# Kernel optimization log

Hardware: AMD Instinct MI355X
Metric: run time of the kernel (lower is better)

Reference implementation:

```python
import jax, jax.numpy as jnp
import numpy as np

H = 8  # num_heads
EPS = 1e-5


def _lin_params(key, din, dout, scale=0.02):
    kw, _ = jax.random.split(key)
    W = jax.random.normal(kw, (din, dout), jnp.float32) * scale
    b = jnp.zeros((dout,), jnp.float32)
    return W, b


def _edge_attention(x_src, x_dst, ei, ea, Wq, bq, Wk, bk, Wv, bv, We, be, Wo, bo, n_dst):
    out_c = Wq.shape[1]
    D = out_c // H
    scale = D ** -0.5
    q = (x_dst @ Wq + bq).reshape(-1, H, D)
    k = (x_src @ Wk + bk).reshape(-1, H, D)
    v = (x_src @ Wv + bv).reshape(-1, H, D)
    e = (ea @ We + be).reshape(-1, H, D)
    src, dst = ei[0], ei[1]
    ke = k[src] + e                                # [E,H,D]
    ve = v[src] + e                                # [E,H,D]
    s = jnp.einsum('ehd,ehd->eh', q[dst], ke) * scale  # [E,H]
    # segment (per-destination) softmax, numerically stable
    m = jax.ops.segment_max(s, dst, num_segments=n_dst)
    ex = jnp.exp(s - m[dst])
    den = jax.ops.segment_sum(ex, dst, num_segments=n_dst)
    a = ex / den[dst]                              # [E,H]  (dropout = identity in eval)
    agg = jax.ops.segment_sum(a[..., None] * ve, dst, num_segments=n_dst)  # [N_dst,H,D]
    return agg.reshape(n_dst, out_c) @ Wo + bo


def _layernorm(x, g, b):
    mu = jnp.mean(x, axis=-1, keepdims=True)
    var = jnp.mean((x - mu) ** 2, axis=-1, keepdims=True)
    return (x - mu) * jax.lax.rsqrt(var + EPS) * g + b


def setup_inputs() -> dict:
    key = jax.random.key(0)
    ks = jax.random.split(key, 32)
    N_pc, N_gr, E_pp, E_pg = 50000, 8000, 400000, 100000
    din, dout, de = 128, 128, 64
    inp = {}
    inp['x_pc'] = jax.random.normal(ks[0], (N_pc, din), jnp.float32)
    inp['x_gr'] = jax.random.normal(ks[1], (N_gr, din), jnp.float32)
    inp['ea_pp'] = jax.random.normal(ks[2], (E_pp, de), jnp.float32)
    inp['ea_pg'] = jax.random.normal(ks[3], (E_pg, de), jnp.float32)
    inp['ei_pp'] = jax.random.randint(ks[4], (2, E_pp), 0, N_pc, jnp.int32)
    src_pg = jax.random.randint(ks[5], (E_pg,), 0, N_pc, jnp.int32)
    dst_pg = jax.random.randint(ks[6], (E_pg,), 0, N_gr, jnp.int32)
    inp['ei_pg'] = jnp.stack([src_pg, dst_pg])
    i = 7
    for et in ('pp', 'pg'):
        for nm, d_in in (('Wq', din), ('Wk', din), ('Wv', din), ('We', de), ('Wo', dout)):
            W, b = _lin_params(ks[i], d_in, dout); i += 1
            inp[f'{nm}_{et}'] = W
            inp[f'b{nm[1].lower()}_{et}'] = b
    for nt, d_in in (('pc', din), ('gr', din)):
        W, b = _lin_params(ks[i], d_in, dout); i += 1
        inp[f'Wnp_{nt}'] = W
        inp[f'bnp_{nt}'] = b
        inp[f'g_{nt}'] = jnp.ones((dout,), jnp.float32)
        inp[f'bln_{nt}'] = jnp.zeros((dout,), jnp.float32)
    return inp


def reference(x_pc, x_gr, ea_pp, ea_pg, ei_pp, ei_pg,
              Wq_pp, bq_pp, Wk_pp, bk_pp, Wv_pp, bv_pp, We_pp, be_pp, Wo_pp, bo_pp,
              Wq_pg, bq_pg, Wk_pg, bk_pg, Wv_pg, bv_pg, We_pg, be_pg, Wo_pg, bo_pg,
              Wnp_pc, bnp_pc, Wnp_gr, bnp_gr, g_pc, bln_pc, g_gr, bln_gr):
    N_pc, N_gr = x_pc.shape[0], x_gr.shape[0]
    out_pc = x_pc @ Wnp_pc + bnp_pc
    out_gr = x_gr @ Wnp_gr + bnp_gr
    out_pc = out_pc + _edge_attention(x_pc, x_pc, ei_pp, ea_pp,
                                      Wq_pp, bq_pp, Wk_pp, bk_pp, Wv_pp, bv_pp,
                                      We_pp, be_pp, Wo_pp, bo_pp, N_pc)
    out_gr = out_gr + _edge_attention(x_pc, x_gr, ei_pg, ea_pg,
                                      Wq_pg, bq_pg, Wk_pg, bk_pg, Wv_pg, bv_pg,
                                      We_pg, be_pg, Wo_pg, bo_pg, N_gr)
    out_pc = _layernorm(out_pc, g_pc, bln_pc)
    out_gr = _layernorm(out_gr, g_gr, bln_gr)
    return out_pc, out_gr
```

## Files before the change

### kernel.cpp

```cpp
#include <hip/hip_runtime.h>
#include <hip/hip_bf16.h>
#include <stdint.h>

typedef short short8 __attribute__((ext_vector_type(8)));
typedef float f32x4 __attribute__((ext_vector_type(4)));

__device__ __forceinline__ unsigned short f2bf(float x) {
    unsigned u = __float_as_uint(x);
    u += 0x7fffu + ((u >> 16) & 1u);
    return (unsigned short)(u >> 16);
}
__device__ __forceinline__ float bflo(unsigned u) { return __uint_as_float(u << 16); }
__device__ __forceinline__ float bfhi(unsigned u) { return __uint_as_float(u & 0xffff0000u); }

struct WDesc { const float* src; unsigned short* dst; int K, ldd, koff, perm; };
struct WPack { WDesc w[12]; };

__global__ __launch_bounds__(256) void prep_and_count(WPack p,
        const int* __restrict__ d0, int E0, int* c0,
        const int* __restrict__ d1, int E1, int* c1, int nPrep) {
    if ((int)blockIdx.x < nPrep) {
        int wi = blockIdx.x >> 2, chunk = blockIdx.x & 3;
        WDesc d = p.w[wi];
        int total = d.K * 128, cs = total >> 2;
        int lo = chunk * cs, hi = lo + cs;
        for (int i = lo + threadIdx.x; i < hi; i += 256) {
            int n = i / d.K, k = i - n * d.K;
            int kk = d.perm ? (2 * (k & 63) + (k >> 6)) : k;
            d.dst[(size_t)n * d.ldd + d.koff + kk] = f2bf(d.src[(size_t)k * 128 + n]);
        }
    } else {
        int t = (blockIdx.x - nPrep) * 256 + threadIdx.x;
        if (t < E0) atomicAdd(&c0[d0[t]], 1);
        else if (t < E0 + E1) atomicAdd(&c1[d1[t - E0]], 1);
    }
}

struct NodeOut { const unsigned short* Wt; const float* bias; unsigned int* out; int ldc, coloff; };
struct NodePack { NodeOut d[5]; int nout; };

__global__ __launch_bounds__(256) void gemm_node(const float* __restrict__ A0, int M0, NodePack p0,
                                                 int B0,
                                                 const float* __restrict__ A1, int M1, NodePack p1) {
    constexpr int K = 128, LDA = 136, LDB = 72, TLD = 133;
    __shared__ __align__(16) unsigned short As[64 * LDA];
    __shared__ __align__(16) unsigned short Bs[128 * LDB];

    const float* A; int M; NodePack dp; int blk;
    if ((int)blockIdx.x < B0) { A = A0; M = M0; dp = p0; blk = blockIdx.x; }
    else { A = A1; M = M1; dp = p1; blk = blockIdx.x - B0; }

    const int tid = threadIdx.x;
    const int rbase = blk * 64;

    for (int slot = tid; slot < 64 * 16; slot += 256) {
        int row = slot >> 4, kg = slot & 15;
        int gr = rbase + row;
        short8 s8 = {0, 0, 0, 0, 0, 0, 0, 0};
        if (gr < M) {
            const float* a = A + (size_t)gr * K + kg * 8;
            float4 f0 = *reinterpret_cast<const float4*>(a);
            float4 f1 = *reinterpret_cast<const float4*>(a + 4);
            s8[0] = (short)f2bf(f0.x); s8[1] = (short)f2bf(f0.y);
            s8[2] = (short)f2bf(f0.z); s8[3] = (short)f2bf(f0.w);
            s8[4] = (short)f2bf(f1.x); s8[5] = (short)f2bf(f1.y);
            s8[6] = (short)f2bf(f1.z); s8[7] = (short)f2bf(f1.w);
        }
        *reinterpret_cast<short8*>(&As[row * LDA + kg * 8]) = s8;
    }

    const int lane = tid & 63, w = tid >> 6;
    const int rb = (w >> 1) * 32, cb = (w & 1) * 64;
    const int qd = lane >> 4, l16 = lane & 15;

    for (int o = 0; o < dp.nout; ++o) {
        NodeOut d = dp.d[o];
        f32x4 acc[2][4];
#pragma unroll
        for (int rt = 0; rt < 2; ++rt)
#pragma unroll
            for (int ct = 0; ct < 4; ++ct) { f32x4 z = {0.f,0.f,0.f,0.f}; acc[rt][ct] = z; }

        for (int kc = 0; kc < K; kc += 64) {
            __syncthreads();
            for (int slot = tid; slot < 128 * 8; slot += 256) {
                int n = slot >> 3, kg = slot & 7;
                *reinterpret_cast<short8*>(&Bs[n * LDB + kg * 8]) =
                    *reinterpret_cast<const short8*>(d.Wt + (size_t)n * K + kc + kg * 8);
            }
            __syncthreads();
#pragma unroll
            for (int ks = 0; ks < 64; ks += 32) {
                short8 af[2], bfr[4];
#pragma unroll
                for (int rt = 0; rt < 2; ++rt)
                    af[rt] = *reinterpret_cast<const short8*>(
                        &As[(rb + rt * 16 + l16) * LDA + kc + ks + qd * 8]);
#pragma unroll
                for (int ct = 0; ct < 4; ++ct)
                    bfr[ct] = *reinterpret_cast<const short8*>(
                        &Bs[(cb + ct * 16 + l16) * LDB + ks + qd * 8]);
#pragma unroll
                for (int rt = 0; rt < 2; ++rt)
#pragma unroll
                    for (int ct = 0; ct < 4; ++ct)
                        acc[rt][ct] = __builtin_amdgcn_mfma_f32_16x16x32_bf16(
                            af[rt], bfr[ct], acc[rt][ct], 0, 0, 0);
            }
        }

        __syncthreads();
        unsigned short* tile = Bs;
#pragma unroll
        for (int ct = 0; ct < 4; ++ct) {
            int col = cb + ct * 16 + l16;
            float bv = d.bias[col];
#pragma unroll
            for (int rt = 0; rt < 2; ++rt)
#pragma unroll
                for (int r = 0; r < 4; ++r)
                    tile[(rb + rt * 16 + qd * 4 + r) * TLD + col] = f2bf(acc[rt][ct][r] + bv);
        }
        __syncthreads();
#pragma unroll
        for (int rep = 0; rep < 4; ++rep) {
            int lrow = (tid >> 4) + rep * 16, seg = tid & 15;
            int gr = rbase + lrow;
            if (gr < M) {
                uint4 pk;
#pragma unroll
                for (int j = 0; j < 4; ++j) {
                    int pcol = seg * 4 + j;
                    unsigned lo16 = tile[lrow * TLD + pcol];
                    unsigned hi16 = tile[lrow * TLD + pcol + 64];
                    ((unsigned*)&pk)[j] = lo16 | (hi16 << 16);
                }
                *reinterpret_cast<uint4*>(&d.out[(size_t)gr * d.ldc + d.coloff + seg * 4]) = pk;
            }
        }
    }
}

struct EdgePack {
    const float* A; const unsigned short* Wt; const float* bias;
    const int* pos; unsigned int* out; int M;
};

__global__ __launch_bounds__(256) void gemm_edge(EdgePack p0, EdgePack p1, int B0) {
    constexpr int LDB = 72;
    __shared__ __align__(16) unsigned short Bs[128 * LDB];

    EdgePack p; int blk;
    if ((int)blockIdx.x < B0) { p = p0; blk = blockIdx.x; } else { p = p1; blk = blockIdx.x - B0; }

    const int tid = threadIdx.x;
    for (int slot = tid; slot < 128 * 8; slot += 256) {
        int n = slot >> 3, k8 = slot & 7;
        *reinterpret_cast<short8*>(&Bs[n * LDB + k8 * 8]) =
            *reinterpret_cast<const short8*>(p.Wt + (size_t)n * 64 + k8 * 8);
    }
    __syncthreads();

    const int lane = tid & 63, w = tid >> 6;
    const int qd = lane >> 4, l16 = lane & 15;
    const int rbase = blk * 128 + w * 32;
    if (rbase >= p.M) return;

    float4 fa[4][2];
#pragma unroll
    for (int rt = 0; rt < 2; ++rt)
#pragma unroll
        for (int ks = 0; ks < 2; ++ks) {
            int gr = rbase + rt * 16 + l16;
            int grc = gr < p.M ? gr : p.M - 1;
            const float* a = p.A + (size_t)grc * 64 + ks * 32 + qd * 8;
            fa[rt * 2 + ks][0] = *reinterpret_cast<const float4*>(a);
            fa[rt * 2 + ks][1] = *reinterpret_cast<const float4*>(a + 4);
        }

    short8 af[2][2];
#pragma unroll
    for (int rt = 0; rt < 2; ++rt)
#pragma unroll
        for (int ks = 0; ks < 2; ++ks) {
            float4 f0 = fa[rt * 2 + ks][0], f1 = fa[rt * 2 + ks][1];
            short8 s;
            s[0] = (short)f2bf(f0.x); s[1] = (short)f2bf(f0.y);
            s[2] = (short)f2bf(f0.z); s[3] = (short)f2bf(f0.w);
            s[4] = (short)f2bf(f1.x); s[5] = (short)f2bf(f1.y);
            s[6] = (short)f2bf(f1.z); s[7] = (short)f2bf(f1.w);
            af[rt][ks] = s;
        }

    f32x4 acc[2][8];
#pragma unroll
    for (int rt = 0; rt < 2; ++rt)
#pragma unroll
        for (int ct = 0; ct < 8; ++ct) { f32x4 z = {0.f,0.f,0.f,0.f}; acc[rt][ct] = z; }
#pragma unroll
    for (int ks = 0; ks < 2; ++ks)
#pragma unroll
        for (int ct = 0; ct < 8; ++ct) {
            short8 bf = *reinterpret_cast<const short8*>(
                &Bs[(ct * 16 + l16) * LDB + ks * 32 + qd * 8]);
            acc[0][ct] = __builtin_amdgcn_mfma_f32_16x16x32_bf16(af[0][ks], bf, acc[0][ct], 0, 0, 0);
            acc[1][ct] = __builtin_amdgcn_mfma_f32_16x16x32_bf16(af[1][ks], bf, acc[1][ct], 0, 0, 0);
        }

    float blo[4], bhi[4];
#pragma unroll
    for (int ct = 0; ct < 4; ++ct) {
        blo[ct] = p.bias[ct * 16 + l16];
        bhi[ct] = p.bias[64 + ct * 16 + l16];
    }
#pragma unroll
    for (int rt = 0; rt < 2; ++rt)
#pragma unroll
        for (int r = 0; r < 4; ++r) {
            int gr = rbase + rt * 16 + qd * 4 + r;
            if (gr < p.M) {
                int dpos = p.pos[gr];
                unsigned int* dst = p.out + (size_t)dpos * 64 + l16;
#pragma unroll
                for (int ct = 0; ct < 4; ++ct) {
                    unsigned lo = f2bf(acc[rt][ct][r] + blo[ct]);
                    unsigned hi = f2bf(acc[rt][ct + 4][r] + bhi[ct]);
                    dst[ct * 16] = lo | (hi << 16);
                }
            }
        }
}

struct OutPack {
    const unsigned short* Aagg; const float* Ax;
    const unsigned short* Wt;
    const float *bo, *bnp, *g, *bln; float* out; int M;
};

__global__ __launch_bounds__(256) void gemm_out_ln(OutPack p0, OutPack p1, int B0) {
    constexpr int K = 256, LDA = 264, LDB = 72, FTLD = 132;
    __shared__ __align__(16) char smemA[64 * LDA * 2];
    __shared__ __align__(16) unsigned short Bs[128 * LDB];
    unsigned short* As = (unsigned short*)smemA;

    OutPack p; int blk;
    if ((int)blockIdx.x < B0) { p = p0; blk = blockIdx.x; } else { p = p1; blk = blockIdx.x - B0; }

    const int tid = threadIdx.x;
    const int rbase = blk * 64;

    for (int slot = tid; slot < 64 * 32; slot += 256) {
        int row = slot >> 5, kg = slot & 31;
        int gr = rbase + row;
        short8 s8 = {0, 0, 0, 0, 0, 0, 0, 0};
        if (gr < p.M) {
            if (kg < 16) {
                s8 = *reinterpret_cast<const short8*>(p.Aagg + (size_t)gr * 128 + kg * 8);
            } else {
                const float* a = p.Ax + (size_t)gr * 128 + (kg - 16) * 8;
                float4 f0 = *reinterpret_cast<const float4*>(a);
                float4 f1 = *reinterpret_cast<const float4*>(a + 4);
                s8[0] = (short)f2bf(f0.x); s8[1] = (short)f2bf(f0.y);
                s8[2] = (short)f2bf(f0.z); s8[3] = (short)f2bf(f0.w);
                s8[4] = (short)f2bf(f1.x); s8[5] = (short)f2bf(f1.y);
                s8[6] = (short)f2bf(f1.z); s8[7] = (short)f2bf(f1.w);
            }
        }
        *reinterpret_cast<short8*>(&As[row * LDA + kg * 8]) = s8;
    }

    const int lane = tid & 63, w = tid >> 6;
    const int rb = (w >> 1) * 32, cb = (w & 1) * 64;
    const int qd = lane >> 4, l16 = lane & 15;

    f32x4 acc[2][4];
#pragma unroll
    for (int rt = 0; rt < 2; ++rt)
#pragma unroll
        for (int ct = 0; ct < 4; ++ct) { f32x4 z = {0.f,0.f,0.f,0.f}; acc[rt][ct] = z; }

    for (int kc = 0; kc < K; kc += 64) {
        __syncthreads();
        for (int slot = tid; slot < 128 * 8; slot += 256) {
            int n = slot >> 3, kg = slot & 7;
            *reinterpret_cast<short8*>(&Bs[n * LDB + kg * 8]) =
                *reinterpret_cast<const short8*>(p.Wt + (size_t)n * K + kc + kg * 8);
        }
        __syncthreads();
#pragma unroll
        for (int ks = 0; ks < 64; ks += 32) {
            short8 af[2], bfr[4];
#pragma unroll
            for (int rt = 0; rt < 2; ++rt)
                af[rt] = *reinterpret_cast<const short8*>(
                    &As[(rb + rt * 16 + l16) * LDA + kc + ks + qd * 8]);
#pragma unroll
            for (int ct = 0; ct < 4; ++ct)
                bfr[ct] = *reinterpret_cast<const short8*>(
                    &Bs[(cb + ct * 16 + l16) * LDB + ks + qd * 8]);
#pragma unroll
            for (int rt = 0; rt < 2; ++rt)
#pragma unroll
                for (int ct = 0; ct < 4; ++ct)
                    acc[rt][ct] = __builtin_amdgcn_mfma_f32_16x16x32_bf16(
                        af[rt], bfr[ct], acc[rt][ct], 0, 0, 0);
        }
    }

    __syncthreads();
    float* ftile = (float*)smemA;
#pragma unroll
    for (int ct = 0; ct < 4; ++ct) {
        int col = cb + ct * 16 + l16;
        float bv = p.bo[col] + p.bnp[col];
#pragma unroll
        for (int rt = 0; rt < 2; ++rt)
#pragma unroll
            for (int r = 0; r < 4; ++r)
                ftile[(rb + rt * 16 + qd * 4 + r) * FTLD + col] = acc[rt][ct][r] + bv;
    }
    __syncthreads();

    int r = tid >> 2, q4 = tid & 3;
    const float* rowp = &ftile[r * FTLD + q4 * 32];
    float s = 0.f, sq = 0.f;
#pragma unroll
    for (int j = 0; j < 8; ++j) {
        float4 v = *reinterpret_cast<const float4*>(rowp + j * 4);
        s += v.x + v.y + v.z + v.w;
        sq += v.x * v.x + v.y * v.y + v.z * v.z + v.w * v.w;
    }
    s += __shfl_xor(s, 1, 64);  s += __shfl_xor(s, 2, 64);
    sq += __shfl_xor(sq, 1, 64); sq += __shfl_xor(sq, 2, 64);
    float mu = s * (1.f / 128.f);
    float var = sq * (1.f / 128.f) - mu * mu;
    float rs = rsqrtf(var + 1e-5f);
    int gr = rbase + r;
    if (gr < p.M) {
#pragma unroll
        for (int j = 0; j < 8; ++j) {
            float4 v = *reinterpret_cast<const float4*>(rowp + j * 4);
            int c = q4 * 32 + j * 4;
            float4 gg = *reinterpret_cast<const float4*>(p.g + c);
            float4 bb = *reinterpret_cast<const float4*>(p.bln + c);
            float4 o;
            o.x = (v.x - mu) * rs * gg.x + bb.x;
            o.y = (v.y - mu) * rs * gg.y + bb.y;
            o.z = (v.z - mu) * rs * gg.z + bb.z;
            o.w = (v.w - mu) * rs * gg.w + bb.w;
            *reinterpret_cast<float4*>(&p.out[(size_t)gr * 128 + c]) = o;
        }
    }
}

__global__ __launch_bounds__(1024) void scan_partial(const int* c0, int N0, int* rp0, int* bs0, int B0,
                                                     const int* c1, int N1, int* rp1, int* bs1) {
    __shared__ int wsum[16];
    const int* c; int* rp; int* bs; int N; int blk;
    if ((int)blockIdx.x < B0) { c = c0; rp = rp0; bs = bs0; N = N0; blk = blockIdx.x; }
    else { c = c1; rp = rp1; bs = bs1; N = N1; blk = blockIdx.x - B0; }
    int tid = threadIdx.x, lane = tid & 63, w = tid >> 6;
    int i = blk * 1024 + tid;
    int v = (i < N) ? c[i] : 0;
    int s = v;
#pragma unroll
    for (int off = 1; off < 64; off <<= 1) {
        int t = __shfl_up(s, off, 64);
        if (lane >= off) s += t;
    }
    if (lane == 63) wsum[w] = s;
    __syncthreads();
    if (w == 0 && lane < 16) {
        int ws = wsum[lane];
#pragma unroll
        for (int off = 1; off < 16; off <<= 1) {
            int t = __shfl_up(ws, off, 64);
            if (lane >= off) ws += t;
        }
        wsum[lane] = ws;
    }
    __syncthreads();
    int wexcl = (w == 0) ? 0 : wsum[w - 1];
    if (i < N) rp[i] = wexcl + s - v;
    if (tid == 0) bs[blk] = wsum[15];
}

__global__ __launch_bounds__(128) void scan_mid(const int* bs0, int* off0, int B0, int* rpN0,
                                                const int* bs1, int* off1, int B1, int* rpN1) {
    int w = threadIdx.x >> 6, lane = threadIdx.x & 63;
    const int* bs = w ? bs1 : bs0;
    int* off = w ? off1 : off0;
    int B = w ? B1 : B0;
    int* rpN = w ? rpN1 : rpN0;
    int v = (lane < B) ? bs[lane] : 0;
    int s = v;
#pragma unroll
    for (int o = 1; o < 64; o <<= 1) {
        int t = __shfl_up(s, o, 64);
        if (lane >= o) s += t;
    }
    if (lane < B) off[lane] = s - v;
    int total = __shfl(s, B - 1, 64);
    if (lane == 0) *rpN = total;
}

__global__ __launch_bounds__(1024) void scan_add(int* rp0, int* cur0, const int* off0, int N0, int B0,
                                                 int* rp1, int* cur1, const int* off1, int N1) {
    int* rp; int* cur; const int* off; int N; int blk;
    if ((int)blockIdx.x < B0) { rp = rp0; cur = cur0; off = off0; N = N0; blk = blockIdx.x; }
    else { rp = rp1; cur = cur1; off = off1; N = N1; blk = blockIdx.x - B0; }
    int i = blk * 1024 + threadIdx.x;
    if (i < N) {
        int vv = rp[i] + off[blk];
        rp[i] = vv;
        cur[i] = vv;
    }
}

__global__ __launch_bounds__(256) void scatter_both(
    const int* __restrict__ s0, const int* __restrict__ d0, int E0, int* cur0, int* pos0, int* srcs0,
    const int* __restrict__ s1, const int* __restrict__ d1, int E1, int* cur1, int* pos1, int* srcs1) {
    int t = blockIdx.x * 256 + threadIdx.x;
    if (t < E0) {
        int p = atomicAdd(&cur0[d0[t]], 1);
        pos0[t] = p;
        srcs0[p] = s0[t];
    } else if (t < E0 + E1) {
        int tt = t - E0;
        int p = atomicAdd(&cur1[d1[tt]], 1);
        pos1[tt] = p;
        srcs1[p] = s1[tt];
    }
}

struct AttnPack {
    const unsigned int *q, *kv, *e;
    const int *srcs;
    const int *row_ptr;
    unsigned int* agg; int N;
};

__global__ __launch_bounds__(256) void attn_gather(AttnPack a0, AttnPack a1, int B0) {
    AttnPack a; int blk;
    if ((int)blockIdx.x < B0) { a = a0; blk = blockIdx.x; } else { a = a1; blk = blockIdx.x - B0; }
    int dst = blk * 4 + (threadIdx.x >> 6);
    if (dst >= a.N) return;
    int lane = threadIdx.x & 63;

    unsigned qp = a.q[(size_t)dst * 64 + lane];
    float qlo = bflo(qp), qhi = bfhi(qp);
    int beg = a.row_ptr[dst], end = a.row_ptr[dst + 1];
    float denl = 0.f, denh = 0.f, accl = 0.f, acch = 0.f;

    int s0 = a.srcs[beg], s1 = a.srcs[beg + 1];
    unsigned k0 = a.kv[(size_t)s0 * 128 + lane];
    unsigned v0 = a.kv[(size_t)s0 * 128 + 64 + lane];
    unsigned e0 = a.e[(size_t)beg * 64 + lane];
    unsigned k1 = a.kv[(size_t)s1 * 128 + lane];
    unsigned v1 = a.kv[(size_t)s1 * 128 + 64 + lane];
    unsigned e1 = a.e[(size_t)(beg + 1) * 64 + lane];

    for (int i = beg; i < end; i += 2) {
        int sn0 = a.srcs[i + 2], sn1 = a.srcs[i + 3];
        unsigned kn0 = a.kv[(size_t)sn0 * 128 + lane];
        unsigned vn0 = a.kv[(size_t)sn0 * 128 + 64 + lane];
        unsigned en0 = a.e[(size_t)(i + 2) * 64 + lane];
        unsigned kn1 = a.kv[(size_t)sn1 * 128 + lane];
        unsigned vn1 = a.kv[(size_t)sn1 * 128 + 64 + lane];
        unsigned en1 = a.e[(size_t)(i + 3) * 64 + lane];

        float e0l = bflo(e0), e0h = bfhi(e0);
        float e1l = bflo(e1), e1h = bfhi(e1);
        float p0l = qlo * (bflo(k0) + e0l), p0h = qhi * (bfhi(k0) + e0h);
        float p1l = qlo * (bflo(k1) + e1l), p1h = qhi * (bfhi(k1) + e1h);
#pragma unroll
        for (int m = 1; m < 16; m <<= 1) {
            p0l += __shfl_xor(p0l, m, 64);
            p0h += __shfl_xor(p0h, m, 64);
            p1l += __shfl_xor(p1l, m, 64);
            p1h += __shfl_xor(p1h, m, 64);
        }
        float x0l = __expf(p0l * 0.25f), x0h = __expf(p0h * 0.25f);
        float x1l = __expf(p1l * 0.25f), x1h = __expf(p1h * 0.25f);
        bool second = (i + 1 < end);
        x1l = second ? x1l : 0.f;
        x1h = second ? x1h : 0.f;
        denl += x0l + x1l;
        denh += x0h + x1h;
        accl += x0l * (bflo(v0) + e0l) + x1l * (bflo(v1) + e1l);
        acch += x0h * (bfhi(v0) + e0h) + x1h * (bfhi(v1) + e1h);
        k0 = kn0; v0 = vn0; e0 = en0;
        k1 = kn1; v1 = vn1; e1 = en1;
    }
    float ol = denl > 0.f ? accl / denl : 0.f;
    float oh = denh > 0.f ? acch / denh : 0.f;
    a.agg[(size_t)dst * 64 + lane] = (unsigned)f2bf(ol) | ((unsigned)f2bf(oh) << 16);
}

extern "C" void kernel_launch(void* const* d_in, const int* in_sizes, int n_in,
                              void* d_out, int out_size, void* d_ws, size_t ws_size,
                              hipStream_t stream) {
    const float* x_pc  = (const float*)d_in[0];
    const float* x_gr  = (const float*)d_in[1];
    const float* ea_pp = (const float*)d_in[2];
    const float* ea_pg = (const float*)d_in[3];
    const int* ei_pp   = (const int*)d_in[4];
    const int* ei_pg   = (const int*)d_in[5];
    const float *Wq_pp = (const float*)d_in[6],  *bq_pp = (const float*)d_in[7];
    const float *Wk_pp = (const float*)d_in[8],  *bk_pp = (const float*)d_in[9];
    const float *Wv_pp = (const float*)d_in[10], *bv_pp = (const float*)d_in[11];
    const float *We_pp = (const float*)d_in[12], *be_pp = (const float*)d_in[13];
    const float *Wo_pp = (const float*)d_in[14], *bo_pp = (const float*)d_in[15];
    const float *Wq_pg = (const float*)d_in[16], *bq_pg = (const float*)d_in[17];
    const float *Wk_pg = (const float*)d_in[18], *bk_pg = (const float*)d_in[19];
    const float *Wv_pg = (const float*)d_in[20], *bv_pg = (const float*)d_in[21];
    const float *We_pg = (const float*)d_in[22], *be_pg = (const float*)d_in[23];
    const float *Wo_pg = (const float*)d_in[24], *bo_pg = (const float*)d_in[25];
    const float *Wnp_pc = (const float*)d_in[26], *bnp_pc = (const float*)d_in[27];
    const float *g_pc   = (const float*)d_in[28], *bln_pc = (const float*)d_in[29];
    const float *Wnp_gr = (const float*)d_in[30], *bnp_gr = (const float*)d_in[31];
    const float *g_gr   = (const float*)d_in[32], *bln_gr = (const float*)d_in[33];

    const int N_pc = in_sizes[0] / 128;
    const int N_gr = in_sizes[1] / 128;
    const int E_pp = in_sizes[4] / 2;
    const int E_pg = in_sizes[5] / 2;

    char* ws = (char*)d_ws;
    size_t off = 0;
    auto alloc = [&](size_t bytes) -> char* {
        char* p = ws + off;
        off += (bytes + 255) & ~(size_t)255;
        return p;
    };
    unsigned short* Wt_q_pp = (unsigned short*)alloc(128 * 128 * 2);
    unsigned short* Wt_k_pp = (unsigned short*)alloc(128 * 128 * 2);
    unsigned short* Wt_v_pp = (unsigned short*)alloc(128 * 128 * 2);
    unsigned short* Wt_k_pg = (unsigned short*)alloc(128 * 128 * 2);
    unsigned short* Wt_v_pg = (unsigned short*)alloc(128 * 128 * 2);
    unsigned short* Wt_q_pg = (unsigned short*)alloc(128 * 128 * 2);
    unsigned short* Wt_e_pp = (unsigned short*)alloc(64 * 128 * 2);
    unsigned short* Wt_e_pg = (unsigned short*)alloc(64 * 128 * 2);
    unsigned short* Wt_cat_pp = (unsigned short*)alloc(256 * 128 * 2);
    unsigned short* Wt_cat_gr = (unsigned short*)alloc(256 * 128 * 2);

    unsigned int* q_pp  = (unsigned int*)alloc((size_t)N_pc * 64 * 4);
    unsigned int* kv_pp = (unsigned int*)alloc((size_t)N_pc * 128 * 4);
    unsigned int* q_pg  = (unsigned int*)alloc((size_t)N_gr * 64 * 4);
    unsigned int* kv_pg = (unsigned int*)alloc((size_t)N_pc * 128 * 4);
    unsigned int* e_pp  = (unsigned int*)alloc((size_t)(E_pp + 4) * 64 * 4);
    unsigned int* e_pg  = (unsigned int*)alloc((size_t)(E_pg + 4) * 64 * 4);
    unsigned int* agg_pp = (unsigned int*)alloc((size_t)N_pc * 64 * 4);
    unsigned int* agg_pg = (unsigned int*)alloc((size_t)N_gr * 64 * 4);
    int* row_ptr_pp = (int*)alloc((size_t)(N_pc + 1) * 4);
    int* cursor_pp  = (int*)alloc((size_t)N_pc * 4);
    int* pos_pp     = (int*)alloc((size_t)E_pp * 4);
    int* row_ptr_pg = (int*)alloc((size_t)(N_gr + 1) * 4);
    int* cursor_pg  = (int*)alloc((size_t)N_gr * 4);
    int* pos_pg     = (int*)alloc((size_t)E_pg * 4);
    int* bsum_pp    = (int*)alloc(64 * 4);
    int* boff_pp    = (int*)alloc(64 * 4);
    int* bsum_pg    = (int*)alloc(64 * 4);
    int* boff_pg    = (int*)alloc(64 * 4);
    char* zbase = ws + off;
    int* counts_pp = (int*)alloc((size_t)N_pc * 4);
    int* counts_pg = (int*)alloc((size_t)N_gr * 4);
    int* srcs_pp   = (int*)alloc((size_t)(E_pp + 8) * 4);
    int* srcs_pg   = (int*)alloc((size_t)(E_pg + 8) * 4);
    size_t zbytes = (size_t)((ws + off) - zbase);
    hipMemsetAsync(zbase, 0, zbytes, stream);
    hipMemsetAsync(e_pp + (size_t)E_pp * 64, 0, 4 * 64 * 4, stream);
    hipMemsetAsync(e_pg + (size_t)E_pg * 64, 0, 4 * 64 * 4, stream);

    float* out_pc = (float*)d_out;
    float* out_gr = out_pc + (size_t)N_pc * 128;

    const int* src_pp = ei_pp;
    const int* dst_pp = ei_pp + E_pp;
    const int* src_pg = ei_pg;
    const int* dst_pg = ei_pg + E_pg;

    WPack wp;
    wp.w[0]  = {Wq_pp, Wt_q_pp, 128, 128, 0, 0};
    wp.w[1]  = {Wk_pp, Wt_k_pp, 128, 128, 0, 0};
    wp.w[2]  = {Wv_pp, Wt_v_pp, 128, 128, 0, 0};
    wp.w[3]  = {Wk_pg, Wt_k_pg, 128, 128, 0, 0};
    wp.w[4]  = {Wv_pg, Wt_v_pg, 128, 128, 0, 0};
    wp.w[5]  = {Wq_pg, Wt_q_pg, 128, 128, 0, 0};
    wp.w[6]  = {We_pp, Wt_e_pp, 64, 64, 0, 0};
    wp.w[7]  = {We_pg, Wt_e_pg, 64, 64, 0, 0};
    wp.w[8]  = {Wo_pp, Wt_cat_pp, 128, 256, 0, 1};
    wp.w[9]  = {Wnp_pc, Wt_cat_pp, 128, 256, 128, 0};
    wp.w[10] = {Wo_pg, Wt_cat_gr, 128, 256, 0, 1};
    wp.w[11] = {Wnp_gr, Wt_cat_gr, 128, 256, 128, 0};
    const int NPREP = 48;
    const int gE = (E_pp + E_pg + 255) / 256;
    prep_and_count<<<NPREP + gE, 256, 0, stream>>>(wp, dst_pp, E_pp, counts_pp,
                                                   dst_pg, E_pg, counts_pg, NPREP);

    const int Bs_pp = (N_pc + 1023) / 1024, Bs_pg = (N_gr + 1023) / 1024;
    scan_partial<<<Bs_pp + Bs_pg, 1024, 0, stream>>>(counts_pp, N_pc, row_ptr_pp, bsum_pp, Bs_pp,
                                                     counts_pg, N_gr, row_ptr_pg, bsum_pg);
    scan_mid<<<1, 128, 0, stream>>>(bsum_pp, boff_pp, Bs_pp, &row_ptr_pp[N_pc],
                                    bsum_pg, boff_pg, Bs_pg, &row_ptr_pg[N_gr]);
    scan_add<<<Bs_pp + Bs_pg, 1024, 0, stream>>>(row_ptr_pp, cursor_pp, boff_pp, N_pc, Bs_pp,
                                                 row_ptr_pg, cursor_pg, boff_pg, N_gr);
    scatter_both<<<gE, 256, 0, stream>>>(src_pp, dst_pp, E_pp, cursor_pp, pos_pp, srcs_pp,
                                         src_pg, dst_pg, E_pg, cursor_pg, pos_pg, srcs_pg);

    NodePack np;
    np.d[0] = {Wt_q_pp, bq_pp, q_pp, 64, 0};
    np.d[1] = {Wt_k_pp, bk_pp, kv_pp, 128, 0};
    np.d[2] = {Wt_v_pp, bv_pp, kv_pp, 128, 64};
    np.d[3] = {Wt_k_pg, bk_pg, kv_pg, 128, 0};
    np.d[4] = {Wt_v_pg, bv_pg, kv_pg, 128, 64};
    np.nout = 5;
    NodePack ng{};
    ng.d[0] = {Wt_q_pg, bq_pg, q_pg, 64, 0};
    ng.nout = 1;
    int Bn0 = (N_pc + 63) / 64, Bn1 = (N_gr + 63) / 64;
    gemm_node<<<Bn0 + Bn1, 256, 0, stream>>>(x_pc, N_pc, np, Bn0, x_gr, N_gr, ng);

    EdgePack ep0 = {ea_pp, Wt_e_pp, be_pp, pos_pp, e_pp, E_pp};
    EdgePack ep1 = {ea_pg, Wt_e_pg, be_pg, pos_pg, e_pg, E_pg};
    int Be0 = (E_pp + 127) / 128, Be1 = (E_pg + 127) / 128;
    gemm_edge<<<Be0 + Be1, 256, 0, stream>>>(ep0, ep1, Be0);

    AttnPack ap0 = {q_pp, kv_pp, e_pp, srcs_pp, row_ptr_pp, agg_pp, N_pc};
    AttnPack ap1 = {q_pg, kv_pg, e_pg, srcs_pg, row_ptr_pg, agg_pg, N_gr};
    int Ba0 = (N_pc + 3) / 4, Ba1 = (N_gr + 3) / 4;
    attn_gather<<<Ba0 + Ba1, 256, 0, stream>>>(ap0, ap1, Ba0);

    OutPack op0 = {(const unsigned short*)agg_pp, x_pc, Wt_cat_pp, bo_pp, bnp_pc, g_pc, bln_pc, out_pc, N_pc};
    OutPack op1 = {(const unsigned short*)agg_pg, x_gr, Wt_cat_gr, bo_pg, bnp_gr, g_gr, bln_gr, out_gr, N_gr};
    int Bo0 = (N_pc + 63) / 64, Bo1 = (N_gr + 63) / 64;
    gemm_out_ln<<<Bo0 + Bo1, 256, 0, stream>>>(op0, op1, Bo0);
}
```

Measured before the change: 523.7 us.

## Merge node and edge projection GEMMs into one launch without shared-memory staging

Replaces the separate node-projection and edge-projection kernels with a single kernel whose blocks are split between edge jobs and node jobs. Both paths now keep A fragments in registers and read bf16 weight fragments straight from global memory (cache) instead of staging them through LDS with barriers. The node path is retiled so each wave owns 32 rows across all 128 output columns. This removes a launch and the sync overhead and lets the two workloads overlap, at the cost of more register pressure and repeated global weight reads per wave, plus uncoalesced node output stores in place of the LDS-transposed vector stores.

```diff
diff --git a/kernel.cpp b/kernel.cpp
--- a/kernel.cpp
+++ b/kernel.cpp
@@ -36,199 +36,146 @@
     }
 }
 
-struct NodeOut { const unsigned short* Wt; const float* bias; unsigned int* out; int ldc, coloff; };
-struct NodePack { NodeOut d[5]; int nout; };
-
-__global__ __launch_bounds__(256) void gemm_node(const float* __restrict__ A0, int M0, NodePack p0,
-                                                 int B0,
-                                                 const float* __restrict__ A1, int M1, NodePack p1) {
-    constexpr int K = 128, LDA = 136, LDB = 72, TLD = 133;
-    __shared__ __align__(16) unsigned short As[64 * LDA];
-    __shared__ __align__(16) unsigned short Bs[128 * LDB];
-
-    const float* A; int M; NodePack dp; int blk;
-    if ((int)blockIdx.x < B0) { A = A0; M = M0; dp = p0; blk = blockIdx.x; }
-    else { A = A1; M = M1; dp = p1; blk = blockIdx.x - B0; }
-
-    const int tid = threadIdx.x;
-    const int rbase = blk * 64;
-
-    for (int slot = tid; slot < 64 * 16; slot += 256) {
-        int row = slot >> 4, kg = slot & 15;
-        int gr = rbase + row;
-        short8 s8 = {0, 0, 0, 0, 0, 0, 0, 0};
-        if (gr < M) {
-            const float* a = A + (size_t)gr * K + kg * 8;
-            float4 f0 = *reinterpret_cast<const float4*>(a);
-            float4 f1 = *reinterpret_cast<const float4*>(a + 4);
-            s8[0] = (short)f2bf(f0.x); s8[1] = (short)f2bf(f0.y);
-            s8[2] = (short)f2bf(f0.z); s8[3] = (short)f2bf(f0.w);
-            s8[4] = (short)f2bf(f1.x); s8[5] = (short)f2bf(f1.y);
-            s8[6] = (short)f2bf(f1.z); s8[7] = (short)f2bf(f1.w);
-        }
-        *reinterpret_cast<short8*>(&As[row * LDA + kg * 8]) = s8;
-    }
-
-    const int lane = tid & 63, w = tid >> 6;
-    const int rb = (w >> 1) * 32, cb = (w & 1) * 64;
-    const int qd = lane >> 4, l16 = lane & 15;
-
-    for (int o = 0; o < dp.nout; ++o) {
-        NodeOut d = dp.d[o];
-        f32x4 acc[2][4];
-#pragma unroll
-        for (int rt = 0; rt < 2; ++rt)
-#pragma unroll
-            for (int ct = 0; ct < 4; ++ct) { f32x4 z = {0.f,0.f,0.f,0.f}; acc[rt][ct] = z; }
-
-        for (int kc = 0; kc < K; kc += 64) {
-            __syncthreads();
-            for (int slot = tid; slot < 128 * 8; slot += 256) {
-                int n = slot >> 3, kg = slot & 7;
-                *reinterpret_cast<short8*>(&Bs[n * LDB + kg * 8]) =
-                    *reinterpret_cast<const short8*>(d.Wt + (size_t)n * K + kc + kg * 8);
-            }
-            __syncthreads();
-#pragma unroll
-            for (int ks = 0; ks < 64; ks += 32) {
-                short8 af[2], bfr[4];
-#pragma unroll
-                for (int rt = 0; rt < 2; ++rt)
-                    af[rt] = *reinterpret_cast<const short8*>(
-                        &As[(rb + rt * 16 + l16) * LDA + kc + ks + qd * 8]);
-#pragma unroll
-                for (int ct = 0; ct < 4; ++ct)
-                    bfr[ct] = *reinterpret_cast<const short8*>(
-                        &Bs[(cb + ct * 16 + l16) * LDB + ks + qd * 8]);
-#pragma unroll
-                for (int rt = 0; rt < 2; ++rt)
-#pragma unroll
-                    for (int ct = 0; ct < 4; ++ct)
-                        acc[rt][ct] = __builtin_amdgcn_mfma_f32_16x16x32_bf16(
-                            af[rt], bfr[ct], acc[rt][ct], 0, 0, 0);
-            }
-        }
-
-        __syncthreads();
-        unsigned short* tile = Bs;
-#pragma unroll
-        for (int ct = 0; ct < 4; ++ct) {
-            int col = cb + ct * 16 + l16;
-            float bv = d.bias[col];
-#pragma unroll
-            for (int rt = 0; rt < 2; ++rt)
-#pragma unroll
-                for (int r = 0; r < 4; ++r)
-                    tile[(rb + rt * 16 + qd * 4 + r) * TLD + col] = f2bf(acc[rt][ct][r] + bv);
-        }
-        __syncthreads();
-#pragma unroll
-        for (int rep = 0; rep < 4; ++rep) {
-            int lrow = (tid >> 4) + rep * 16, seg = tid & 15;
-            int gr = rbase + lrow;
-            if (gr < M) {
-                uint4 pk;
-#pragma unroll
-                for (int j = 0; j < 4; ++j) {
-                    int pcol = seg * 4 + j;
-                    unsigned lo16 = tile[lrow * TLD + pcol];
-                    unsigned hi16 = tile[lrow * TLD + pcol + 64];
-                    ((unsigned*)&pk)[j] = lo16 | (hi16 << 16);
-                }
-                *reinterpret_cast<uint4*>(&d.out[(size_t)gr * d.ldc + d.coloff + seg * 4]) = pk;
-            }
-        }
-    }
-}
-
-struct EdgePack {
+struct ProjDesc { const unsigned short* Wt; const float* bias; unsigned int* out; int ldc, coloff; };
+struct NodeJob { const float* A; int M; int nout; ProjDesc d[5]; };
+struct EdgeJob {
     const float* A; const unsigned short* Wt; const float* bias;
     const int* pos; unsigned int* out; int M;
 };
 
-__global__ __launch_bounds__(256) void gemm_edge(EdgePack p0, EdgePack p1, int B0) {
-    constexpr int LDB = 72;
-    __shared__ __align__(16) unsigned short Bs[128 * LDB];
-
-    EdgePack p; int blk;
-    if ((int)blockIdx.x < B0) { p = p0; blk = blockIdx.x; } else { p = p1; blk = blockIdx.x - B0; }
-
+__global__ __launch_bounds__(256) void gemm_ne(EdgeJob e0, EdgeJob e1, NodeJob n0, NodeJob n1,
+                                               int BE0, int BE1, int BN0) {
     const int tid = threadIdx.x;
-    for (int slot = tid; slot < 128 * 8; slot += 256) {
-        int n = slot >> 3, k8 = slot & 7;
-        *reinterpret_cast<short8*>(&Bs[n * LDB + k8 * 8]) =
-            *reinterpret_cast<const short8*>(p.Wt + (size_t)n * 64 + k8 * 8);
-    }
-    __syncthreads();
-
     const int lane = tid & 63, w = tid >> 6;
     const int qd = lane >> 4, l16 = lane & 15;
-    const int rbase = blk * 128 + w * 32;
-    if (rbase >= p.M) return;
-
-    float4 fa[4][2];
-#pragma unroll
-    for (int rt = 0; rt < 2; ++rt)
-#pragma unroll
-        for (int ks = 0; ks < 2; ++ks) {
-            int gr = rbase + rt * 16 + l16;
-            int grc = gr < p.M ? gr : p.M - 1;
-            const float* a = p.A + (size_t)grc * 64 + ks * 32 + qd * 8;
-            fa[rt * 2 + ks][0] = *reinterpret_cast<const float4*>(a);
-            fa[rt * 2 + ks][1] = *reinterpret_cast<const float4*>(a + 4);
-        }
-
-    short8 af[2][2];
-#pragma unroll
-    for (int rt = 0; rt < 2; ++rt)
-#pragma unroll
-        for (int ks = 0; ks < 2; ++ks) {
-            float4 f0 = fa[rt * 2 + ks][0], f1 = fa[rt * 2 + ks][1];
-            short8 s;
-            s[0] = (short)f2bf(f0.x); s[1] = (short)f2bf(f0.y);
-            s[2] = (short)f2bf(f0.z); s[3] = (short)f2bf(f0.w);
-            s[4] = (short)f2bf(f1.x); s[5] = (short)f2bf(f1.y);
-            s[6] = (short)f2bf(f1.z); s[7] = (short)f2bf(f1.w);
-            af[rt][ks] = s;
-        }
-
-    f32x4 acc[2][8];
-#pragma unroll
-    for (int rt = 0; rt < 2; ++rt)
-#pragma unroll
-        for (int ct = 0; ct < 8; ++ct) { f32x4 z = {0.f,0.f,0.f,0.f}; acc[rt][ct] = z; }
-#pragma unroll
-    for (int ks = 0; ks < 2; ++ks)
-#pragma unroll
-        for (int ct = 0; ct < 8; ++ct) {
-            short8 bf = *reinterpret_cast<const short8*>(
-                &Bs[(ct * 16 + l16) * LDB + ks * 32 + qd * 8]);
-            acc[0][ct] = __builtin_amdgcn_mfma_f32_16x16x32_bf16(af[0][ks], bf, acc[0][ct], 0, 0, 0);
-            acc[1][ct] = __builtin_amdgcn_mfma_f32_16x16x32_bf16(af[1][ks], bf, acc[1][ct], 0, 0, 0);
-        }
-
-    float blo[4], bhi[4];
-#pragma unroll
-    for (int ct = 0; ct < 4; ++ct) {
-        blo[ct] = p.bias[ct * 16 + l16];
-        bhi[ct] = p.bias[64 + ct * 16 + l16];
-    }
-#pragma unroll
-    for (int rt = 0; rt < 2; ++rt)
-#pragma unroll
-        for (int r = 0; r < 4; ++r) {
-            int gr = rbase + rt * 16 + qd * 4 + r;
-            if (gr < p.M) {
-                int dpos = p.pos[gr];
-                unsigned int* dst = p.out + (size_t)dpos * 64 + l16;
-#pragma unroll
-                for (int ct = 0; ct < 4; ++ct) {
-                    unsigned lo = f2bf(acc[rt][ct][r] + blo[ct]);
-                    unsigned hi = f2bf(acc[rt][ct + 4][r] + bhi[ct]);
-                    dst[ct * 16] = lo | (hi << 16);
+    int b = blockIdx.x;
+
+    if (b < BE0 + BE1) {
+        EdgeJob p; int blk;
+        if (b < BE0) { p = e0; blk = b; } else { p = e1; blk = b - BE0; }
+        const int rbase = blk * 128 + w * 32;
+        if (rbase >= p.M) return;
+
+        short8 af[2][2];
+#pragma unroll
+        for (int rt = 0; rt < 2; ++rt)
+#pragma unroll
+            for (int ks = 0; ks < 2; ++ks) {
+                int gr = rbase + rt * 16 + l16;
+                int grc = gr < p.M ? gr : p.M - 1;
+                const float* a = p.A + (size_t)grc * 64 + ks * 32 + qd * 8;
+                float4 f0 = *reinterpret_cast<const float4*>(a);
+                float4 f1 = *reinterpret_cast<const float4*>(a + 4);
+                short8 s;
+                s[0] = (short)f2bf(f0.x); s[1] = (short)f2bf(f0.y);
+                s[2] = (short)f2bf(f0.z); s[3] = (short)f2bf(f0.w);
+                s[4] = (short)f2bf(f1.x); s[5] = (short)f2bf(f1.y);
+                s[6] = (short)f2bf(f1.z); s[7] = (short)f2bf(f1.w);
+                af[rt][ks] = s;
+            }
+
+        f32x4 acc[2][8];
+#pragma unroll
+        for (int rt = 0; rt < 2; ++rt)
+#pragma unroll
+            for (int ct = 0; ct < 8; ++ct) { f32x4 z = {0.f,0.f,0.f,0.f}; acc[rt][ct] = z; }
+#pragma unroll
+        for (int ks = 0; ks < 2; ++ks)
+#pragma unroll
+            for (int ct = 0; ct < 8; ++ct) {
+                short8 bf = *reinterpret_cast<const short8*>(
+                    p.Wt + (size_t)(ct * 16 + l16) * 64 + ks * 32 + qd * 8);
+                acc[0][ct] = __builtin_amdgcn_mfma_f32_16x16x32_bf16(af[0][ks], bf, acc[0][ct], 0, 0, 0);
+                acc[1][ct] = __builtin_amdgcn_mfma_f32_16x16x32_bf16(af[1][ks], bf, acc[1][ct], 0, 0, 0);
+            }
+
+        float blo[4], bhi[4];
+#pragma unroll
+        for (int ct = 0; ct < 4; ++ct) {
+            blo[ct] = p.bias[ct * 16 + l16];
+            bhi[ct] = p.bias[64 + ct * 16 + l16];
+        }
+#pragma unroll
+        for (int rt = 0; rt < 2; ++rt)
+#pragma unroll
+            for (int r = 0; r < 4; ++r) {
+                int gr = rbase + rt * 16 + qd * 4 + r;
+                if (gr < p.M) {
+                    int dpos = p.pos[gr];
+                    unsigned int* dst = p.out + (size_t)dpos * 64 + l16;
+#pragma unroll
+                    for (int ct = 0; ct < 4; ++ct) {
+                        unsigned lo = f2bf(acc[rt][ct][r] + blo[ct]);
+                        unsigned hi = f2bf(acc[rt][ct + 4][r] + bhi[ct]);
+                        dst[ct * 16] = lo | (hi << 16);
+                    }
                 }
             }
-        }
+    } else {
+        NodeJob p; int blk;
+        int bb = b - BE0 - BE1;
+        if (bb < BN0) { p = n0; blk = bb; } else { p = n1; blk = bb - BN0; }
+        const int rbase = blk * 128 + w * 32;
+        if (rbase >= p.M) return;
+
+        short8 af[2][4];
+#pragma unroll
+        for (int rt = 0; rt < 2; ++rt)
+#pragma unroll
+            for (int ks = 0; ks < 4; ++ks) {
+                int gr = rbase + rt * 16 + l16;
+                int grc = gr < p.M ? gr : p.M - 1;
+                const float* a = p.A + (size_t)grc * 128 + ks * 32 + qd * 8;
+                float4 f0 = *reinterpret_cast<const float4*>(a);
+                float4 f1 = *reinterpret_cast<const float4*>(a + 4);
+                short8 s;
+                s[0] = (short)f2bf(f0.x); s[1] = (short)f2bf(f0.y);
+                s[2] = (short)f2bf(f0.z); s[3] = (short)f2bf(f0.w);
+                s[4] = (short)f2bf(f1.x); s[5] = (short)f2bf(f1.y);
+                s[6] = (short)f2bf(f1.z); s[7] = (short)f2bf(f1.w);
+                af[rt][ks] = s;
+            }
+
+        for (int o = 0; o < p.nout; ++o) {
+            ProjDesc d = p.d[o];
+            f32x4 acc[2][8];
+#pragma unroll
+            for (int rt = 0; rt < 2; ++rt)
+#pragma unroll
+                for (int ct = 0; ct < 8; ++ct) { f32x4 z = {0.f,0.f,0.f,0.f}; acc[rt][ct] = z; }
+#pragma unroll
+            for (int ks = 0; ks < 4; ++ks)
+#pragma unroll
+                for (int ct = 0; ct < 8; ++ct) {
+                    short8 bf = *reinterpret_cast<const short8*>(
+                        d.Wt + (size_t)(ct * 16 + l16) * 128 + ks * 32 + qd * 8);
+                    acc[0][ct] = __builtin_amdgcn_mfma_f32_16x16x32_bf16(af[0][ks], bf, acc[0][ct], 0, 0, 0);
+                    acc[1][ct] = __builtin_amdgcn_mfma_f32_16x16x32_bf16(af[1][ks], bf, acc[1][ct], 0, 0, 0);
+                }
+
+            float blo[4], bhi[4];
+#pragma unroll
+            for (int ct = 0; ct < 4; ++ct) {
+                blo[ct] = d.bias[ct * 16 + l16];
+                bhi[ct] = d.bias[64 + ct * 16 + l16];
+            }
+#pragma unroll
+            for (int rt = 0; rt < 2; ++rt)
+#pragma unroll
+                for (int r = 0; r < 4; ++r) {
+                    int gr = rbase + rt * 16 + qd * 4 + r;
+                    if (gr < p.M) {
+                        unsigned int* dst = d.out + (size_t)gr * d.ldc + d.coloff + l16;
+#pragma unroll
+                        for (int ct = 0; ct < 4; ++ct) {
+                            unsigned lo = f2bf(acc[rt][ct][r] + blo[ct]);
+                            unsigned hi = f2bf(acc[rt][ct + 4][r] + bhi[ct]);
+                            dst[ct * 16] = lo | (hi << 16);
+                        }
+                    }
+                }
+        }
+    }
 }
 
 struct OutPack {
@@ -608,23 +555,21 @@
     scatter_both<<<gE, 256, 0, stream>>>(src_pp, dst_pp, E_pp, cursor_pp, pos_pp, srcs_pp,
                                          src_pg, dst_pg, E_pg, cursor_pg, pos_pg, srcs_pg);
 
-    NodePack np;
-    np.d[0] = {Wt_q_pp, bq_pp, q_pp, 64, 0};
-    np.d[1] = {Wt_k_pp, bk_pp, kv_pp, 128, 0};
-    np.d[2] = {Wt_v_pp, bv_pp, kv_pp, 128, 64};
-    np.d[3] = {Wt_k_pg, bk_pg, kv_pg, 128, 0};
-    np.d[4] = {Wt_v_pg, bv_pg, kv_pg, 128, 64};
-    np.nout = 5;
-    NodePack ng{};
-    ng.d[0] = {Wt_q_pg, bq_pg, q_pg, 64, 0};
-    ng.nout = 1;
-    int Bn0 = (N_pc + 63) / 64, Bn1 = (N_gr + 63) / 64;
-    gemm_node<<<Bn0 + Bn1, 256, 0, stream>>>(x_pc, N_pc, np, Bn0, x_gr, N_gr, ng);
-
-    EdgePack ep0 = {ea_pp, Wt_e_pp, be_pp, pos_pp, e_pp, E_pp};
-    EdgePack ep1 = {ea_pg, Wt_e_pg, be_pg, pos_pg, e_pg, E_pg};
-    int Be0 = (E_pp + 127) / 128, Be1 = (E_pg + 127) / 128;
-    gemm_edge<<<Be0 + Be1, 256, 0, stream>>>(ep0, ep1, Be0);
+    EdgeJob ej0 = {ea_pp, Wt_e_pp, be_pp, pos_pp, e_pp, E_pp};
+    EdgeJob ej1 = {ea_pg, Wt_e_pg, be_pg, pos_pg, e_pg, E_pg};
+    NodeJob nj0{};
+    nj0.A = x_pc; nj0.M = N_pc; nj0.nout = 5;
+    nj0.d[0] = {Wt_q_pp, bq_pp, q_pp, 64, 0};
+    nj0.d[1] = {Wt_k_pp, bk_pp, kv_pp, 128, 0};
+    nj0.d[2] = {Wt_v_pp, bv_pp, kv_pp, 128, 64};
+    nj0.d[3] = {Wt_k_pg, bk_pg, kv_pg, 128, 0};
+    nj0.d[4] = {Wt_v_pg, bv_pg, kv_pg, 128, 64};
+    NodeJob nj1{};
+    nj1.A = x_gr; nj1.M = N_gr; nj1.nout = 1;
+    nj1.d[0] = {Wt_q_pg, bq_pg, q_pg, 64, 0};
+    int BE0 = (E_pp + 127) / 128, BE1 = (E_pg + 127) / 128;
+    int BN0 = (N_pc + 127) / 128, BN1 = (N_gr + 127) / 128;
+    gemm_ne<<<BE0 + BE1 + BN0 + BN1, 256, 0, stream>>>(ej0, ej1, nj0, nj1, BE0, BE1, BN0);
 
     AttnPack ap0 = {q_pp, kv_pp, e_pp, srcs_pp, row_ptr_pp, agg_pp, N_pc};
     AttnPack ap1 = {q_pg, kv_pg, e_pg, srcs_pg, row_ptr_pg, agg_pg, N_gr};
```

Measured after the change: 542.1 us. +3.5%, slower.
